# Kernel optimization log

Measured on AMD Instinct MI355X. Metric: run time of the kernel, lower is better.

The kernel has to match this reference:

```python
import jax, jax.numpy as jnp
import numpy as np

TEMPERATURES = (0.1, 0.5, 1.0)
B, Q, P, N, D = 1024, 128, 32, 128, 64


def _cdist(a, b):
    # Euclidean pairwise distance, matching torch.cdist(p=2): [B,Q,D]x[B,K,D]->[B,Q,K]
    a2 = jnp.sum(a * a, axis=-1, keepdims=True)            # [B,Q,1]
    b2 = jnp.sum(b * b, axis=-1, keepdims=True)            # [B,K,1]
    d2 = a2 + jnp.swapaxes(b2, -1, -2) - 2.0 * jnp.einsum('bqd,bkd->bqk', a, b)
    return jnp.sqrt(jnp.maximum(d2, 0.0))


def _conditioned_V(x, y_pos, y_neg, temperature):
    n_neg = y_neg.shape[1]
    dist_pos = _cdist(x, y_pos)                            # [B,Q,P]
    dist_neg = _cdist(x, y_neg)                            # [B,Q,N]
    dist = jnp.concatenate([dist_neg, dist_pos], axis=-1)  # [B,Q,N+P]
    log_kernel = jnp.maximum(-dist / temperature, -80.0)
    kernel = jnp.exp(log_kernel)
    row_sum = jnp.sum(kernel, axis=-1, keepdims=True)      # [B,Q,1]
    col_sum = jnp.sum(kernel, axis=-2, keepdims=True)      # [B,1,N+P]
    normalizer = jnp.sqrt(jnp.maximum(row_sum * col_sum, 1e-12))
    affinity = kernel / normalizer
    affinity_neg = affinity[:, :, :n_neg]
    affinity_pos = affinity[:, :, n_neg:]
    weight_pos = affinity_pos * jnp.sum(affinity_neg, axis=-1, keepdims=True)
    weight_neg = affinity_neg * jnp.sum(affinity_pos, axis=-1, keepdims=True)
    drift = (jnp.einsum('bqp,bpd->bqd', weight_pos, y_pos)
             - jnp.einsum('bqn,bnd->bqd', weight_neg, y_neg))
    return drift


def setup_inputs() -> dict:
    key = jax.random.key(0)
    kx, kp, kn = jax.random.split(key, 3)
    return {
        'x': jax.random.normal(kx, (B, Q, D), dtype=jnp.float32),
        'y_pos': jax.random.normal(kp, (B, P, D), dtype=jnp.float32),
        'y_neg': jax.random.normal(kn, (B, N, D), dtype=jnp.float32),
    }


def reference(x, y_pos, y_neg):
    # mean cross distance (no grad in original -> stop_gradient)
    mean_dist = jax.lax.stop_gradient(jnp.mean(_cdist(x, y_pos)))
    drift_total = jnp.zeros_like(x)
    for base_t in TEMPERATURES:  # small fixed loop over temperatures, as in source
        adaptive_t = jax.lax.stop_gradient(jnp.maximum(base_t * mean_dist, 1e-6))
        drift_total = drift_total + _conditioned_V(x, y_pos, y_neg, adaptive_t)
    target = jax.lax.stop_gradient(x + drift_total)
    loss = jnp.mean((x - target) ** 2)
    return loss
```

## Files before the change

kernel.cpp:

```cpp
#include <hip/hip_runtime.h>

namespace {
constexpr int B = 1024, Q = 128, P = 32, N = 128, D = 64, K = 160;

__global__ __launch_bounds__(256) void k_meandist(
    const float* __restrict__ x, const float* __restrict__ y_pos,
    double* __restrict__ ws) {
  __shared__ float Yp[P][D];
  __shared__ float ysq[P];
  __shared__ float red[4];
  const int b = blockIdx.x, tid = threadIdx.x;
  const float* yb = y_pos + (size_t)b * P * D;
  for (int i = tid; i < P * D / 4; i += 256)
    reinterpret_cast<float4*>(&Yp[0][0])[i] = reinterpret_cast<const float4*>(yb)[i];
  __syncthreads();
  if (tid < P) {
    float s = 0.f;
    for (int d = 0; d < D; ++d) { float v = Yp[tid][d]; s = fmaf(v, v, s); }
    ysq[tid] = s;
  }
  __syncthreads();
  const int q = tid >> 1, ph = tid & 1;
  const float* xq = x + ((size_t)b * Q + q) * D;
  float acc[16];
#pragma unroll
  for (int j = 0; j < 16; ++j) acc[j] = 0.f;
  float xsq = 0.f;
#pragma unroll 1
  for (int d4 = 0; d4 < 16; ++d4) {
    float4 xv = reinterpret_cast<const float4*>(xq)[d4];
    xsq = fmaf(xv.x, xv.x, fmaf(xv.y, xv.y, fmaf(xv.z, xv.z, fmaf(xv.w, xv.w, xsq))));
#pragma unroll
    for (int j = 0; j < 16; ++j) {
      float4 yv = reinterpret_cast<const float4*>(&Yp[ph * 16 + j][0])[d4];
      acc[j] = fmaf(xv.x, yv.x, fmaf(xv.y, yv.y, fmaf(xv.z, yv.z, fmaf(xv.w, yv.w, acc[j]))));
    }
  }
  float dsum = 0.f;
#pragma unroll
  for (int j = 0; j < 16; ++j) {
    float d2 = xsq + ysq[ph * 16 + j] - 2.f * acc[j];
    dsum += sqrtf(fmaxf(d2, 0.f));
  }
#pragma unroll
  for (int m = 1; m < 64; m <<= 1) dsum += __shfl_xor(dsum, m);
  if ((tid & 63) == 0) red[tid >> 6] = dsum;
  __syncthreads();
  if (tid == 0)
    atomicAdd(ws, (double)(red[0] + red[1] + red[2] + red[3]));
}

__global__
__attribute__((amdgpu_flat_work_group_size(1024, 1024)))
__attribute__((amdgpu_waves_per_eu(2, 4)))
void k_drift3(
    const float* __restrict__ x, const float* __restrict__ y_pos,
    const float* __restrict__ y_neg, double* __restrict__ ws) {
  __shared__ __align__(16) float SM[33160];
  float4* Y4  = (float4*)SM;
  float4* X4c = (float4*)(SM + 10240);
  float*  Cs  = SM + 10240;
  float4* C4  = (float4*)(SM + 10240);
  float* rss = SM + 31360;
  float* css = SM + 31744;
  float* uss = SM + 32224;
  float* vss = SM + 32608;
  float* ysq = SM + 32992;
  double* redd = (double*)(SM + 33152);

  const int b = blockIdx.x, tid = threadIdx.x;
  const float4* yn4 = (const float4*)(y_neg + (size_t)b * N * D);
  const float4* yp4 = (const float4*)(y_pos + (size_t)b * P * D);
  const float4* xg  = (const float4*)(x + (size_t)b * Q * D);

  for (int idx = tid; idx < K * 16; idx += 1024) {
    int k = idx >> 4, d4 = idx & 15;
    float4 v = (k < N) ? yn4[k * 16 + d4] : yp4[(k - N) * 16 + d4];
    Y4[k * 16 + ((d4 + k) & 15)] = v;
  }
  if (tid < 384) { rss[tid] = 0.f; uss[tid] = 0.f; vss[tid] = 0.f; }
  __syncthreads();
  if (tid < K) {
    float s = 0.f;
#pragma unroll
    for (int c = 0; c < 16; ++c) {
      float4 v = Y4[tid * 16 + ((c + tid) & 15)];
      s = fmaf(v.x, v.x, fmaf(v.y, v.y, fmaf(v.z, v.z, fmaf(v.w, v.w, s))));
    }
    ysq[tid] = s;
  }

  const int qg = tid & 31, kt = tid >> 5;
  const int qb = qg * 4;

  float zz[4][5], xs4[4];
#pragma unroll
  for (int i = 0; i < 4; ++i) {
    xs4[i] = 0.f;
#pragma unroll
    for (int j = 0; j < 5; ++j) zz[i][j] = 0.f;
  }

#pragma unroll 1
  for (int ch = 0; ch < 2; ++ch) {
    if (ch) __syncthreads();
    {
      int q = tid >> 3, c = tid & 7;
      X4c[q * 8 + ((c + (q >> 2)) & 7)] = xg[q * 16 + ch * 8 + c];
    }
    __syncthreads();
#pragma unroll 2
    for (int d4 = 0; d4 < 8; ++d4) {
      const int gd4 = ch * 8 + d4;
      const int rx = (d4 + qg) & 7;
      float4 xv[4];
#pragma unroll
      for (int i = 0; i < 4; ++i) xv[i] = X4c[(qb + i) * 8 + rx];
#pragma unroll
      for (int i = 0; i < 4; ++i)
        xs4[i] = fmaf(xv[i].x, xv[i].x, fmaf(xv[i].y, xv[i].y,
                 fmaf(xv[i].z, xv[i].z, fmaf(xv[i].w, xv[i].w, xs4[i]))));
#pragma unroll
      for (int j = 0; j < 5; ++j) {
        const int k_ = kt + 32 * j;
        float4 yv = Y4[k_ * 16 + ((gd4 + k_) & 15)];
#pragma unroll
        for (int i = 0; i < 4; ++i)
          zz[i][j] = fmaf(xv[i].x, yv.x, fmaf(xv[i].y, yv.y,
                     fmaf(xv[i].z, yv.z, fmaf(xv[i].w, yv.w, zz[i][j]))));
      }
    }
  }

  const float meand = (float)(ws[0] * (1.0 / ((double)B * Q * P)));
  const float invt2 = 1.0f / fmaxf(meand, 1e-6f);
#pragma unroll
  for (int i = 0; i < 4; ++i)
#pragma unroll
    for (int j = 0; j < 5; ++j) {
      const int k_ = kt + 32 * j;
      float d2 = xs4[i] + ysq[k_] - 2.f * zz[i][j];
      zz[i][j] = __expf(-sqrtf(fmaxf(d2, 0.f)) * invt2);
    }

#pragma unroll
  for (int t = 0; t < 3; ++t) {
    float ers[4] = {0.f, 0.f, 0.f, 0.f};
    float ecs[5] = {0.f, 0.f, 0.f, 0.f, 0.f};
#pragma unroll
    for (int i = 0; i < 4; ++i)
#pragma unroll
      for (int j = 0; j < 5; ++j) {
        float z = zz[i][j], f;
        if (t == 2) f = z;
        else if (t == 1) f = z * z;
        else { float z2 = z * z, z4 = z2 * z2; f = z4 * z4 * z2; }
        ers[i] += f; ecs[j] += f;
      }
#pragma unroll
    for (int j = 0; j < 5; ++j) {
      float v = ecs[j];
      v += __shfl_xor(v, 1); v += __shfl_xor(v, 2);
      v += __shfl_xor(v, 4); v += __shfl_xor(v, 8); v += __shfl_xor(v, 16);
      if (qg == 0) css[t * 160 + kt + 32 * j] = v;
    }
#pragma unroll
    for (int i = 0; i < 4; ++i) {
      float v = ers[i];
      v += __shfl_xor(v, 32);
      if ((tid & 63) < 32) atomicAdd(&rss[t * 128 + qb + i], v);
    }
  }
  __syncthreads();
  if (tid < 480) css[tid] = rsqrtf(css[tid]);
  __syncthreads();

#pragma unroll
  for (int t = 0; t < 3; ++t) {
    float icr[5];
#pragma unroll
    for (int j = 0; j < 5; ++j) icr[j] = css[t * 160 + kt + 32 * j];
    float uu[4] = {0.f, 0.f, 0.f, 0.f};
    float vv[4] = {0.f, 0.f, 0.f, 0.f};
#pragma unroll
    for (int i = 0; i < 4; ++i)
#pragma unroll
      for (int j = 0; j < 5; ++j) {
        float z = zz[i][j], f;
        if (t == 2) f = z;
        else if (t == 1) f = z * z;
        else { float z2 = z * z, z4 = z2 * z2; f = z4 * z4 * z2; }
        float a = f * icr[j];
        if (j == 4) uu[i] += a; else vv[i] += a;
      }
#pragma unroll
    for (int i = 0; i < 4; ++i) {
      float u = uu[i]; u += __shfl_xor(u, 32);
      float v = vv[i]; v += __shfl_xor(v, 32);
      if ((tid & 63) < 32) {
        atomicAdd(&uss[t * 128 + qb + i], u);
        atomicAdd(&vss[t * 128 + qb + i], v);
      }
    }
  }
  __syncthreads();
  if (tid < 384) {
    float inv = 1.0f / rss[tid];
    uss[tid] *= inv;
    vss[tid] *= inv;
  }
  __syncthreads();

  {
    float ic0a[5], ic1a[5], ic2a[5];
#pragma unroll
    for (int j = 0; j < 5; ++j) {
      const int k_ = kt + 32 * j;
      ic0a[j] = css[k_]; ic1a[j] = css[160 + k_]; ic2a[j] = css[320 + k_];
    }
#pragma unroll
    for (int i = 0; i < 4; ++i) {
      const int q2 = qb + i;
      float u0 = uss[q2], u1 = uss[128 + q2], u2 = uss[256 + q2];
      float v0 = vss[q2], v1 = vss[128 + q2], v2 = vss[256 + q2];
#pragma unroll
      for (int j = 0; j < 5; ++j) {
        const int k_ = kt + 32 * j;
        const bool pos = (j == 4);
        float a0 = pos ? v0 : u0, a1 = pos ? v1 : u1, a2 = pos ? v2 : u2;
        float z = zz[i][j], z2 = z * z, z4 = z2 * z2, z10 = z4 * z4 * z2;
        float c = fmaf(z, ic2a[j] * a2, fmaf(z2, ic1a[j] * a1, z10 * (ic0a[j] * a0)));
        Cs[k_ * 132 + q2] = pos ? c : -c;
      }
    }
  }
  __syncthreads();

  const int kc = tid >> 8, qc = (tid >> 3) & 31, dc = tid & 7;
  float dr[4][8];
#pragma unroll
  for (int i = 0; i < 4; ++i)
#pragma unroll
    for (int n = 0; n < 8; ++n) dr[i][n] = 0.f;

#pragma unroll 4
  for (int kk = 0; kk < 40; ++kk) {
    const int k_ = kc * 40 + kk;
    float4 ca = C4[k_ * 33 + qc];
    float4 y0 = Y4[k_ * 16 + ((2 * dc + k_) & 15)];
    float4 y1 = Y4[k_ * 16 + ((2 * dc + 1 + k_) & 15)];
#define GACC(ii, cv)                               \
    dr[ii][0] = fmaf(cv, y0.x, dr[ii][0]);         \
    dr[ii][1] = fmaf(cv, y0.y, dr[ii][1]);         \
    dr[ii][2] = fmaf(cv, y0.z, dr[ii][2]);         \
    dr[ii][3] = fmaf(cv, y0.w, dr[ii][3]);         \
    dr[ii][4] = fmaf(cv, y1.x, dr[ii][4]);         \
    dr[ii][5] = fmaf(cv, y1.y, dr[ii][5]);         \
    dr[ii][6] = fmaf(cv, y1.z, dr[ii][6]);         \
    dr[ii][7] = fmaf(cv, y1.w, dr[ii][7]);
    GACC(0, ca.x) GACC(1, ca.y) GACC(2, ca.z) GACC(3, ca.w)
#undef GACC
  }
  __syncthreads();

  float4* FB = Y4;
  const int c0 = (2 * dc + qc) & 15, c1 = (2 * dc + 1 + qc) & 15;
  if (kc > 0) {
    const int off = (kc - 1) * 2048;
#pragma unroll
    for (int i = 0; i < 4; ++i) {
      const int q = qc * 4 + i;
      FB[off + q * 16 + c0] = make_float4(dr[i][0], dr[i][1], dr[i][2], dr[i][3]);
      FB[off + q * 16 + c1] = make_float4(dr[i][4], dr[i][5], dr[i][6], dr[i][7]);
    }
  }
  __syncthreads();
  if (kc == 0) {
    float tot = 0.f;
#pragma unroll
    for (int i = 0; i < 4; ++i) {
      const int q = qc * 4 + i;
      float4 s0 = FB[q * 16 + c0];
      float4 t0 = FB[2048 + q * 16 + c0];
      float4 u0 = FB[4096 + q * 16 + c0];
      float a0 = dr[i][0] + s0.x + t0.x + u0.x;
      float a1 = dr[i][1] + s0.y + t0.y + u0.y;
      float a2 = dr[i][2] + s0.z + t0.z + u0.z;
      float a3 = dr[i][3] + s0.w + t0.w + u0.w;
      tot = fmaf(a0, a0, tot); tot = fmaf(a1, a1, tot);
      tot = fmaf(a2, a2, tot); tot = fmaf(a3, a3, tot);
      float4 s1 = FB[q * 16 + c1];
      float4 t1 = FB[2048 + q * 16 + c1];
      float4 u1 = FB[4096 + q * 16 + c1];
      float a4 = dr[i][4] + s1.x + t1.x + u1.x;
      float a5 = dr[i][5] + s1.y + t1.y + u1.y;
      float a6 = dr[i][6] + s1.z + t1.z + u1.z;
      float a7 = dr[i][7] + s1.w + t1.w + u1.w;
      tot = fmaf(a4, a4, tot); tot = fmaf(a5, a5, tot);
      tot = fmaf(a6, a6, tot); tot = fmaf(a7, a7, tot);
    }
#pragma unroll
    for (int m = 1; m < 64; m <<= 1) tot += __shfl_xor(tot, m);
    if ((tid & 63) == 0) redd[tid >> 6] = (double)tot;
  }
  __syncthreads();
  if (tid == 0)
    atomicAdd(ws + 1, redd[0] + redd[1] + redd[2] + redd[3]);
}

__global__ void k_final(const double* __restrict__ ws, float* __restrict__ out) {
  out[0] = (float)(ws[1] / ((double)B * Q * D));
}

}

extern "C" void kernel_launch(void* const* d_in, const int* in_sizes, int n_in,
                              void* d_out, int out_size, void* d_ws, size_t ws_size,
                              hipStream_t stream) {
  const float* x = (const float*)d_in[0];
  const float* y_pos = (const float*)d_in[1];
  const float* y_neg = (const float*)d_in[2];
  float* out = (float*)d_out;
  double* ws = (double*)d_ws;

  hipMemsetAsync(d_ws, 0, 2 * sizeof(double), stream);
  k_meandist<<<B, 256, 0, stream>>>(x, y_pos, ws);
  k_drift3<<<B, 1024, 0, stream>>>(x, y_pos, y_neg, ws);
  k_final<<<1, 1, 0, stream>>>(ws, out);
}
```

Before: 267.6 us.

## Stream coefficient matrix through smaller LDS chunks to allow two blocks per CU

```diff
diff --git a/kernel.cpp b/kernel.cpp
--- a/kernel.cpp
+++ b/kernel.cpp
@@ -52,21 +52,20 @@
 
 __global__
 __attribute__((amdgpu_flat_work_group_size(1024, 1024)))
-__attribute__((amdgpu_waves_per_eu(2, 4)))
-void k_drift3(
+__attribute__((amdgpu_waves_per_eu(2, 8)))
+void k_drift4(
     const float* __restrict__ x, const float* __restrict__ y_pos,
     const float* __restrict__ y_neg, double* __restrict__ ws) {
-  __shared__ __align__(16) float SM[33160];
+  __shared__ __align__(16) float SM[17328];
   float4* Y4  = (float4*)SM;
   float4* X4c = (float4*)(SM + 10240);
-  float*  Cs  = SM + 10240;
-  float4* C4  = (float4*)(SM + 10240);
-  float* rss = SM + 31360;
-  float* css = SM + 31744;
-  float* uss = SM + 32224;
-  float* vss = SM + 32608;
-  float* ysq = SM + 32992;
-  double* redd = (double*)(SM + 33152);
+  float4* C4s = (float4*)(SM + 10240);
+  float* rss = SM + 15520;
+  float* css = SM + 15904;
+  float* uss = SM + 16384;
+  float* vss = SM + 16768;
+  float* ysq = SM + 17152;
+  double* redd = (double*)(SM + 17312);
 
   const int b = blockIdx.x, tid = threadIdx.x;
   const float4* yn4 = (const float4*)(y_neg + (size_t)b * N * D);
@@ -79,16 +78,6 @@
     Y4[k * 16 + ((d4 + k) & 15)] = v;
   }
   if (tid < 384) { rss[tid] = 0.f; uss[tid] = 0.f; vss[tid] = 0.f; }
-  __syncthreads();
-  if (tid < K) {
-    float s = 0.f;
-#pragma unroll
-    for (int c = 0; c < 16; ++c) {
-      float4 v = Y4[tid * 16 + ((c + tid) & 15)];
-      s = fmaf(v.x, v.x, fmaf(v.y, v.y, fmaf(v.z, v.z, fmaf(v.w, v.w, s))));
-    }
-    ysq[tid] = s;
-  }
 
   const int qg = tid & 31, kt = tid >> 5;
   const int qb = qg * 4;
@@ -103,12 +92,21 @@
 
 #pragma unroll 1
   for (int ch = 0; ch < 2; ++ch) {
-    if (ch) __syncthreads();
+    __syncthreads();
     {
       int q = tid >> 3, c = tid & 7;
       X4c[q * 8 + ((c + (q >> 2)) & 7)] = xg[q * 16 + ch * 8 + c];
     }
     __syncthreads();
+    if (ch == 0 && tid < K) {
+      float s = 0.f;
+#pragma unroll
+      for (int c = 0; c < 16; ++c) {
+        float4 v = Y4[tid * 16 + ((c + tid) & 15)];
+        s = fmaf(v.x, v.x, fmaf(v.y, v.y, fmaf(v.z, v.z, fmaf(v.w, v.w, s))));
+      }
+      ysq[tid] = s;
+    }
 #pragma unroll 2
     for (int d4 = 0; d4 < 8; ++d4) {
       const int gd4 = ch * 8 + d4;
@@ -209,69 +207,72 @@
     uss[tid] *= inv;
     vss[tid] *= inv;
   }
-  __syncthreads();
-
-  {
-    float ic0a[5], ic1a[5], ic2a[5];
+
+  const int kc = tid >> 9, qc = (tid >> 4) & 31, dcc = tid & 15;
+  float dr[4][4];
+#pragma unroll
+  for (int i = 0; i < 4; ++i)
+#pragma unroll
+    for (int n = 0; n < 4; ++n) dr[i][n] = 0.f;
+
+#pragma unroll 1
+  for (int s = 0; s < 4; ++s) {
+    __syncthreads();
 #pragma unroll
     for (int j = 0; j < 5; ++j) {
-      const int k_ = kt + 32 * j;
-      ic0a[j] = css[k_]; ic1a[j] = css[160 + k_]; ic2a[j] = css[320 + k_];
-    }
-#pragma unroll
-    for (int i = 0; i < 4; ++i) {
-      const int q2 = qb + i;
-      float u0 = uss[q2], u1 = uss[128 + q2], u2 = uss[256 + q2];
-      float v0 = vss[q2], v1 = vss[128 + q2], v2 = vss[256 + q2];
-#pragma unroll
-      for (int j = 0; j < 5; ++j) {
+      const int klocal = kt + 32 * j - 40 * s;
+      if (klocal >= 0 && klocal < 40) {
         const int k_ = kt + 32 * j;
         const bool pos = (j == 4);
-        float a0 = pos ? v0 : u0, a1 = pos ? v1 : u1, a2 = pos ? v2 : u2;
-        float z = zz[i][j], z2 = z * z, z4 = z2 * z2, z10 = z4 * z4 * z2;
-        float c = fmaf(z, ic2a[j] * a2, fmaf(z2, ic1a[j] * a1, z10 * (ic0a[j] * a0)));
-        Cs[k_ * 132 + q2] = pos ? c : -c;
-      }
-    }
-  }
-  __syncthreads();
-
-  const int kc = tid >> 8, qc = (tid >> 3) & 31, dc = tid & 7;
-  float dr[4][8];
-#pragma unroll
-  for (int i = 0; i < 4; ++i)
-#pragma unroll
-    for (int n = 0; n < 8; ++n) dr[i][n] = 0.f;
-
+        const float ic0 = css[k_], ic1 = css[160 + k_], ic2 = css[320 + k_];
+        float c0a[4];
+#pragma unroll
+        for (int i = 0; i < 4; ++i) {
+          const int q2 = qb + i;
+          float a0 = pos ? vss[q2]       : uss[q2];
+          float a1 = pos ? vss[128 + q2] : uss[128 + q2];
+          float a2 = pos ? vss[256 + q2] : uss[256 + q2];
+          float z = zz[i][j], z2 = z * z, z4 = z2 * z2, z10 = z4 * z4 * z2;
+          float c = fmaf(z, ic2 * a2, fmaf(z2, ic1 * a1, z10 * (ic0 * a0)));
+          c0a[i] = pos ? c : -c;
+        }
+        C4s[klocal * 33 + qg] = make_float4(c0a[0], c0a[1], c0a[2], c0a[3]);
+      }
+    }
+    __syncthreads();
 #pragma unroll 4
-  for (int kk = 0; kk < 40; ++kk) {
-    const int k_ = kc * 40 + kk;
-    float4 ca = C4[k_ * 33 + qc];
-    float4 y0 = Y4[k_ * 16 + ((2 * dc + k_) & 15)];
-    float4 y1 = Y4[k_ * 16 + ((2 * dc + 1 + k_) & 15)];
-#define GACC(ii, cv)                               \
-    dr[ii][0] = fmaf(cv, y0.x, dr[ii][0]);         \
-    dr[ii][1] = fmaf(cv, y0.y, dr[ii][1]);         \
-    dr[ii][2] = fmaf(cv, y0.z, dr[ii][2]);         \
-    dr[ii][3] = fmaf(cv, y0.w, dr[ii][3]);         \
-    dr[ii][4] = fmaf(cv, y1.x, dr[ii][4]);         \
-    dr[ii][5] = fmaf(cv, y1.y, dr[ii][5]);         \
-    dr[ii][6] = fmaf(cv, y1.z, dr[ii][6]);         \
-    dr[ii][7] = fmaf(cv, y1.w, dr[ii][7]);
-    GACC(0, ca.x) GACC(1, ca.y) GACC(2, ca.z) GACC(3, ca.w)
-#undef GACC
+    for (int kl = 0; kl < 20; ++kl) {
+      const int klocal = kc * 20 + kl;
+      const int k_ = 40 * s + klocal;
+      float4 ca = C4s[klocal * 33 + qc];
+      float4 y0 = Y4[k_ * 16 + ((dcc + k_) & 15)];
+      dr[0][0] = fmaf(ca.x, y0.x, dr[0][0]);
+      dr[0][1] = fmaf(ca.x, y0.y, dr[0][1]);
+      dr[0][2] = fmaf(ca.x, y0.z, dr[0][2]);
+      dr[0][3] = fmaf(ca.x, y0.w, dr[0][3]);
+      dr[1][0] = fmaf(ca.y, y0.x, dr[1][0]);
+      dr[1][1] = fmaf(ca.y, y0.y, dr[1][1]);
+      dr[1][2] = fmaf(ca.y, y0.z, dr[1][2]);
+      dr[1][3] = fmaf(ca.y, y0.w, dr[1][3]);
+      dr[2][0] = fmaf(ca.z, y0.x, dr[2][0]);
+      dr[2][1] = fmaf(ca.z, y0.y, dr[2][1]);
+      dr[2][2] = fmaf(ca.z, y0.z, dr[2][2]);
+      dr[2][3] = fmaf(ca.z, y0.w, dr[2][3]);
+      dr[3][0] = fmaf(ca.w, y0.x, dr[3][0]);
+      dr[3][1] = fmaf(ca.w, y0.y, dr[3][1]);
+      dr[3][2] = fmaf(ca.w, y0.z, dr[3][2]);
+      dr[3][3] = fmaf(ca.w, y0.w, dr[3][3]);
+    }
   }
   __syncthreads();
 
   float4* FB = Y4;
-  const int c0 = (2 * dc + qc) & 15, c1 = (2 * dc + 1 + qc) & 15;
-  if (kc > 0) {
-    const int off = (kc - 1) * 2048;
+  if (kc == 1) {
 #pragma unroll
     for (int i = 0; i < 4; ++i) {
       const int q = qc * 4 + i;
-      FB[off + q * 16 + c0] = make_float4(dr[i][0], dr[i][1], dr[i][2], dr[i][3]);
-      FB[off + q * 16 + c1] = make_float4(dr[i][4], dr[i][5], dr[i][6], dr[i][7]);
+      FB[q * 16 + ((dcc + q) & 15)] =
+          make_float4(dr[i][0], dr[i][1], dr[i][2], dr[i][3]);
     }
   }
   __syncthreads();
@@ -280,32 +281,25 @@
 #pragma unroll
     for (int i = 0; i < 4; ++i) {
       const int q = qc * 4 + i;
-      float4 s0 = FB[q * 16 + c0];
-      float4 t0 = FB[2048 + q * 16 + c0];
-      float4 u0 = FB[4096 + q * 16 + c0];
-      float a0 = dr[i][0] + s0.x + t0.x + u0.x;
-      float a1 = dr[i][1] + s0.y + t0.y + u0.y;
-      float a2 = dr[i][2] + s0.z + t0.z + u0.z;
-      float a3 = dr[i][3] + s0.w + t0.w + u0.w;
+      float4 v = FB[q * 16 + ((dcc + q) & 15)];
+      float a0 = dr[i][0] + v.x;
+      float a1 = dr[i][1] + v.y;
+      float a2 = dr[i][2] + v.z;
+      float a3 = dr[i][3] + v.w;
       tot = fmaf(a0, a0, tot); tot = fmaf(a1, a1, tot);
       tot = fmaf(a2, a2, tot); tot = fmaf(a3, a3, tot);
-      float4 s1 = FB[q * 16 + c1];
-      float4 t1 = FB[2048 + q * 16 + c1];
-      float4 u1 = FB[4096 + q * 16 + c1];
-      float a4 = dr[i][4] + s1.x + t1.x + u1.x;
-      float a5 = dr[i][5] + s1.y + t1.y + u1.y;
-      float a6 = dr[i][6] + s1.z + t1.z + u1.z;
-      float a7 = dr[i][7] + s1.w + t1.w + u1.w;
-      tot = fmaf(a4, a4, tot); tot = fmaf(a5, a5, tot);
-      tot = fmaf(a6, a6, tot); tot = fmaf(a7, a7, tot);
     }
 #pragma unroll
     for (int m = 1; m < 64; m <<= 1) tot += __shfl_xor(tot, m);
     if ((tid & 63) == 0) redd[tid >> 6] = (double)tot;
   }
   __syncthreads();
-  if (tid == 0)
-    atomicAdd(ws + 1, redd[0] + redd[1] + redd[2] + redd[3]);
+  if (tid == 0) {
+    double sT = 0.0;
+#pragma unroll
+    for (int w = 0; w < 8; ++w) sT += redd[w];
+    atomicAdd(ws + 1, sT);
+  }
 }
 
 __global__ void k_final(const double* __restrict__ ws, float* __restrict__ out) {
@@ -325,6 +319,6 @@
 
   hipMemsetAsync(d_ws, 0, 2 * sizeof(double), stream);
   k_meandist<<<B, 256, 0, stream>>>(x, y_pos, ws);
-  k_drift3<<<B, 1024, 0, stream>>>(x, y_pos, y_neg, ws);
+  k_drift4<<<B, 1024, 0, stream>>>(x, y_pos, y_neg, ws);
   k_final<<<1, 1, 0, stream>>>(ws, out);
 }
```

Result: slower. 278.9 us (+4.2%).
